# Performance work log

Hardware: AMD Instinct MI355X
Metric: run time of the kernel (lower is better)

## Reference

```python
import jax, jax.numpy as jnp
import numpy as np

WIN = (7, 7)
SHIFT = (3, 3)
HEADS = 12


def _rel_index():
    wh, ww = WIN
    coords = np.stack(np.meshgrid(np.arange(wh), np.arange(ww), indexing='ij')).reshape(2, -1)
    rel = (coords[:, :, None] - coords[:, None, :]).transpose(1, 2, 0).astype(np.int64)
    rel[:, :, 0] += wh - 1
    rel[:, :, 1] += ww - 1
    rel[:, :, 0] *= 2 * ww - 1
    return rel.sum(-1).reshape(-1)  # [N*N]


def _attn_mask(pH, pW, sh, sw):
    wh, ww = WIN
    mask = np.zeros((pH, pW), np.float32)
    h_sl = [(0, pH - wh), (pH - wh, pH - sh), (pH - sh, pH)]
    w_sl = [(0, pW - ww), (pW - ww, pW - sw), (pW - sw, pW)]
    cnt = 0
    for hs in h_sl:
        for ws in w_sl:
            mask[hs[0]:hs[1], ws[0]:ws[1]] = cnt
            cnt += 1
    nw = (pH // wh) * (pW // ww)
    mask = mask.reshape(pH // wh, wh, pW // ww, ww).transpose(0, 2, 1, 3).reshape(nw, wh * ww)
    diff = mask[:, None, :] - mask[:, :, None]
    return jnp.asarray(np.where(diff != 0, -100.0, 0.0).astype(np.float32))  # [nw, N, N]


def setup_inputs() -> dict:
    key = jax.random.key(0)
    ks = jax.random.split(key, 6)
    C = 384
    return {
        'x': jax.random.normal(ks[0], (16, 56, 56, C), jnp.float32),
        'qkv_weight': jax.random.normal(ks[1], (3 * C, C), jnp.float32) * 0.02,
        'qkv_bias': jax.random.normal(ks[2], (3 * C,), jnp.float32) * 0.02,
        'proj_weight': jax.random.normal(ks[3], (C, C), jnp.float32) * 0.02,
        'proj_bias': jax.random.normal(ks[4], (C,), jnp.float32) * 0.02,
        'rel_table': jax.random.normal(ks[5], (169, HEADS), jnp.float32) * 0.02,
    }


def reference(x, qkv_weight, qkv_bias, proj_weight, proj_bias, rel_table):
    B, H, W, C = x.shape
    wh, ww = WIN
    pad_b = (wh - H % wh) % wh
    pad_r = (ww - W % ww) % ww
    xp = jnp.pad(x, ((0, 0), (0, pad_b), (0, pad_r), (0, 0)))
    pH, pW = H + pad_b, W + pad_r
    sh = 0 if wh >= pH else SHIFT[0]
    sw = 0 if ww >= pW else SHIFT[1]
    shifted = (sh + sw) > 0
    if shifted:
        xp = jnp.roll(xp, (-sh, -sw), axis=(1, 2))
    nwh, nww = pH // wh, pW // ww
    nw, N = nwh * nww, wh * ww
    # window partition -> [B*nw, N, C]
    xw = xp.reshape(B, nwh, wh, nww, ww, C).transpose(0, 1, 3, 2, 4, 5).reshape(B * nw, N, C)
    qkv = xw @ qkv_weight.T + qkv_bias
    qkv = qkv.reshape(B * nw, N, 3, HEADS, C // HEADS).transpose(2, 0, 3, 1, 4)
    q, k, v = qkv[0], qkv[1], qkv[2]  # [B*nw, heads, N, hd]
    q = q * (C // HEADS) ** -0.5
    attn = jnp.einsum('whnd,whmd->whnm', q, k)
    bias = rel_table[jnp.asarray(_rel_index())].reshape(N, N, HEADS).transpose(2, 0, 1)
    attn = attn + bias[None]
    if shifted:
        mask = _attn_mask(pH, pW, sh, sw)  # [nw, N, N]
        attn = (attn.reshape(B, nw, HEADS, N, N) + mask[None, :, None]).reshape(B * nw, HEADS, N, N)
    attn = jax.nn.softmax(attn, axis=-1)
    out = jnp.einsum('whnm,whmd->whnd', attn, v).transpose(0, 2, 1, 3).reshape(B * nw, N, C)
    out = out @ proj_weight.T + proj_bias
    out = out.reshape(B, nwh, nww, wh, ww, C).transpose(0, 1, 3, 2, 4, 5).reshape(B, pH, pW, C)
    if shifted:
        out = jnp.roll(out, (sh, sw), axis=(1, 2))
    return out[:, :H, :W, :]
```

## Files before the change

kernel.cpp:

```cpp
#include <hip/hip_runtime.h>

#define CCH 384
#define NHEADS 12
#define HDIM 32
#define NTOK 49
#define NWIN 1024
#define MROWS 50176
#define PSTR 72

typedef __attribute__((ext_vector_type(8))) short bf16x8;
typedef __attribute__((ext_vector_type(4))) float f32x4;

#define WAITVM_BAR(N) asm volatile("s_waitcnt vmcnt(" #N ")\n\ts_barrier" ::: "memory")
#define BAR() asm volatile("s_barrier" ::: "memory")

__device__ __forceinline__ unsigned short f2bf(float f) {
    unsigned u = __builtin_bit_cast(unsigned, f);
    u += 0x7FFFu + ((u >> 16) & 1u);
    return (unsigned short)(u >> 16);
}

__device__ __forceinline__ void g2lds16(const unsigned short* g, unsigned short* l) {
    __builtin_amdgcn_global_load_lds(
        (const __attribute__((address_space(1))) unsigned int*)g,
        (__attribute__((address_space(3))) unsigned int*)l,
        16, 0, 0);
}

__global__ void prep_kernel(const float* __restrict__ qkvw, const float* __restrict__ projw,
                            const float* __restrict__ rel_table,
                            unsigned short* __restrict__ wq, unsigned short* __restrict__ wp,
                            float* __restrict__ btt2) {
    int i = blockIdx.x * 256 + threadIdx.x;
    if (i < 3 * CCH * CCH) wq[i] = f2bf(qkvw[i]);
    if (i < CCH * CCH) wp[i] = f2bf(projw[i]);
    if (i < 4 * NHEADS * 16 * 64) {
        int cls = i / (NHEADS * 16 * 64);
        int rem = i - cls * (NHEADS * 16 * 64);
        int h = rem / (16 * 64);
        int rem2 = rem - h * (16 * 64);
        int rb = rem2 >> 6, cj = rem2 & 63;
        int jreg = 0;
        if (cj < NTOK) {
            int jy = cj / 7, jx = cj - jy * 7;
            int ry = (cls & 2) ? ((jy < 4) ? 1 : 2) : 0;
            int rx = (cls & 1) ? ((jx < 4) ? 1 : 2) : 0;
            jreg = ry * 3 + rx;
        }
        float4 o;
        float* po = (float*)&o;
#pragma unroll
        for (int rr = 0; rr < 4; ++rr) {
            int ri = rb * 4 + rr;
            float v = -1e30f;
            if (ri < NTOK && cj < NTOK) {
                int iy = ri / 7, ix = ri - iy * 7;
                int jy = cj / 7, jx = cj - jy * 7;
                int idx = (iy - jy + 6) * 13 + (ix - jx + 6);
                v = rel_table[idx * NHEADS + h];
                int ry = (cls & 2) ? ((iy < 4) ? 1 : 2) : 0;
                int rx = (cls & 1) ? ((ix < 4) ? 1 : 2) : 0;
                if (ry * 3 + rx != jreg) v -= 100.f;
            }
            po[rr] = v;
        }
        *(float4*)&btt2[(size_t)i * 4] = o;
    }
}

__device__ __forceinline__ size_t row_to_pixel(int r) {
    int wlin = r / 49, n = r - wlin * 49;
    int b = wlin >> 6, wimg = wlin & 63;
    int wy = wimg >> 3, wx = wimg & 7;
    int iy = n / 7, ix = n - iy * 7;
    int y = wy * 7 + iy + 3; if (y >= 56) y -= 56;
    int x = wx * 7 + ix + 3; if (x >= 56) x -= 56;
    return (size_t)((b * 56 + y) * 56 + x);
}

__global__ __launch_bounds__(256) void gather_kernel(const float* __restrict__ xin,
                                                     unsigned short* __restrict__ xw) {
    int idx = blockIdx.x * 256 + threadIdx.x;
    int row = idx / 96, c4 = (idx - row * 96) * 4;
    const float4 v = *(const float4*)(xin + row_to_pixel(row) * CCH + c4);
    ushort4 o;
    o.x = f2bf(v.x); o.y = f2bf(v.y); o.z = f2bf(v.z); o.w = f2bf(v.w);
    *(ushort4*)(xw + (size_t)row * CCH + c4) = o;
}

__global__ __launch_bounds__(512) void qkv_gemm(const unsigned short* __restrict__ xw,
        const unsigned short* __restrict__ wq, const float* __restrict__ qkv_bias,
        unsigned short* __restrict__ qb, unsigned short* __restrict__ kb,
        unsigned short* __restrict__ vb) {
    __shared__ unsigned short As[2][256 * 32];
    __shared__ unsigned short Bs[2][128 * 32];
    const int tid = threadIdx.x;
    const int bid = blockIdx.x;
    const int xcd = bid & 7;
    const int base = (xcd < 4) ? xcd * 221 : (4 * 221 + (xcd - 4) * 220);
    const int swz = base + (bid >> 3);
    const int rb = swz / 9, cb = swz - rb * 9;
    const int row0 = rb * 256;
    const int col0 = cb * 128;
    const int lane = tid & 63, wv = tid >> 6;
    const int wm = wv >> 1, wn = wv & 1;
    const int l15 = lane & 15, g = lane >> 4;

    const int lrow = lane >> 2;
    const int scs = (lane & 3) * 8;
    const unsigned short* gA0 = xw + (size_t)(row0 + wv * 32 + lrow) * CCH + scs;
    const unsigned short* gA1 = gA0 + (size_t)16 * CCH;
    const unsigned short* gB0 = wq + (size_t)(col0 + wv * 16 + lrow) * CCH + scs;

    f32x4 acc[4][4];
#pragma unroll
    for (int i = 0; i < 4; ++i)
#pragma unroll
        for (int j = 0; j < 4; ++j) acc[i][j] = (f32x4){0.f, 0.f, 0.f, 0.f};

    g2lds16(gA0, &As[0][wv * 1024]);
    g2lds16(gA1, &As[0][wv * 1024 + 512]);
    g2lds16(gB0, &Bs[0][wv * 512]);

#pragma unroll
    for (int kk = 0; kk < 12; ++kk) {
        const int cur = kk & 1;
        if (kk < 11) {
            const int nxt = cur ^ 1;
            g2lds16(gA0 + (kk + 1) * 32, &As[nxt][wv * 1024]);
            g2lds16(gA1 + (kk + 1) * 32, &As[nxt][wv * 1024 + 512]);
            g2lds16(gB0 + (kk + 1) * 32, &Bs[nxt][wv * 512]);
            WAITVM_BAR(3);
        } else {
            WAITVM_BAR(0);
        }
        bf16x8 af[4], bfv[4];
#pragma unroll
        for (int mt = 0; mt < 4; ++mt)
            af[mt] = *(const bf16x8*)&As[cur][(wm * 64 + mt * 16 + l15) * 32 + g * 8];
#pragma unroll
        for (int nt = 0; nt < 4; ++nt)
            bfv[nt] = *(const bf16x8*)&Bs[cur][(wn * 64 + nt * 16 + l15) * 32 + g * 8];
#pragma unroll
        for (int mt = 0; mt < 4; ++mt)
#pragma unroll
            for (int nt = 0; nt < 4; ++nt)
                acc[mt][nt] = __builtin_amdgcn_mfma_f32_16x16x32_bf16(af[mt], bfv[nt], acc[mt][nt], 0, 0, 0);
        BAR();
    }

    const float SCALE = 0.17677669529663687f;
#pragma unroll
    for (int nt = 0; nt < 4; ++nt) {
        int col = col0 + wn * 64 + nt * 16 + l15;
        float bias = qkv_bias[col];
        int which = col / CCH;
        int rem = col - which * CCH;
        int h = rem >> 5, d = rem & 31;
        unsigned short* dstb = (which == 0) ? qb : ((which == 1) ? kb : vb);
        float scl = (which == 0) ? SCALE : 1.0f;
#pragma unroll
        for (int mt = 0; mt < 4; ++mt) {
#pragma unroll
            for (int rr = 0; rr < 4; ++rr) {
                int row = row0 + wm * 64 + mt * 16 + g * 4 + rr;
                int w2 = row / 49, n2 = row - w2 * 49;
                size_t inst = (size_t)(w2 * NHEADS + h);
                float v = (acc[mt][nt][rr] + bias) * scl;
                dstb[(inst * NTOK + n2) * HDIM + d] = f2bf(v);
            }
        }
    }
}

__global__ __launch_bounds__(256) void attn_kernel(const unsigned short* __restrict__ qbuf,
        const unsigned short* __restrict__ kbuf, const unsigned short* __restrict__ vbuf,
        const float* __restrict__ btt2, unsigned short* __restrict__ ao) {
    __shared__ unsigned short Ps[4][64 * PSTR];
    __shared__ unsigned short Vt[4][32 * 64];
    const int tid = threadIdx.x;
    const int lane = tid & 63, wv = tid >> 6;
    const int inst = blockIdx.x * 4 + wv;
    const int w = inst / NHEADS, h = inst - w * NHEADS;
    const int l15 = lane & 15, g = lane >> 4;
    const unsigned short* qp = qbuf + (size_t)inst * (NTOK * HDIM);
    const unsigned short* kp = kbuf + (size_t)inst * (NTOK * HDIM);
    const unsigned short* vp = vbuf + (size_t)inst * (NTOK * HDIM);

    const bf16x8 zero8 = {0, 0, 0, 0, 0, 0, 0, 0};
    bf16x8 vpre[4];
#pragma unroll
    for (int p = 0; p < 4; ++p) {
        int e0 = (p * 64 + lane) * 8;
        int tok = e0 >> 5;
        vpre[p] = (tok < NTOK) ? *(const bf16x8*)&vp[e0] : zero8;
    }

    bf16x8 aq[4], bk[4];
#pragma unroll
    for (int mt = 0; mt < 4; ++mt) {
        int row = mt * 16 + l15;
        aq[mt] = (row < NTOK) ? *(const bf16x8*)&qp[row * HDIM + g * 8] : zero8;
    }
#pragma unroll
    for (int nt = 0; nt < 4; ++nt) {
        int colk = nt * 16 + l15;
        bk[nt] = (colk < NTOK) ? *(const bf16x8*)&kp[colk * HDIM + g * 8] : zero8;
    }
    f32x4 s[4][4];
#pragma unroll
    for (int mt = 0; mt < 4; ++mt)
#pragma unroll
        for (int nt = 0; nt < 4; ++nt)
            s[mt][nt] = __builtin_amdgcn_mfma_f32_16x16x32_bf16(aq[mt], bk[nt], (f32x4){0.f, 0.f, 0.f, 0.f}, 0, 0, 0);

    {
        unsigned short* vt = Vt[wv];
#pragma unroll
        for (int p = 0; p < 4; ++p) {
            int e0 = (p * 64 + lane) * 8;
            int tok = e0 >> 5, d0 = e0 & 31;
#pragma unroll
            for (int j = 0; j < 8; ++j) {
                int d = d0 + j;
                vt[d * 64 + (tok ^ ((d & 7) << 3))] = (unsigned short)vpre[p][j];
            }
        }
    }

    const int wimg = w & 63;
    const int wy = wimg >> 3, wx = wimg & 7;
    const int wcls = (((wy == 7) ? 2 : 0) | ((wx == 7) ? 1 : 0));
    const float4* bt4 = (const float4*)btt2 + ((size_t)(wcls * NHEADS + h)) * (16 * 64);

    float inv[4][4];
#pragma unroll
    for (int mt = 0; mt < 4; ++mt) {
        float4 bias4[4];
#pragma unroll
        for (int nt = 0; nt < 4; ++nt)
            bias4[nt] = bt4[(mt * 4 + g) * 64 + nt * 16 + l15];
#pragma unroll
        for (int rr = 0; rr < 4; ++rr) {
#pragma unroll
            for (int nt = 0; nt < 4; ++nt) {
                float bb = (rr == 0) ? bias4[nt].x : (rr == 1) ? bias4[nt].y : (rr == 2) ? bias4[nt].z : bias4[nt].w;
                s[mt][nt][rr] += bb;
            }
            float m = fmaxf(fmaxf(s[mt][0][rr], s[mt][1][rr]), fmaxf(s[mt][2][rr], s[mt][3][rr]));
            m = fmaxf(m, __shfl_xor(m, 1));
            m = fmaxf(m, __shfl_xor(m, 2));
            m = fmaxf(m, __shfl_xor(m, 4));
            m = fmaxf(m, __shfl_xor(m, 8));
            float sum = 0.f;
#pragma unroll
            for (int nt = 0; nt < 4; ++nt) {
                float p = __expf(s[mt][nt][rr] - m);
                s[mt][nt][rr] = p;
                sum += p;
            }
            sum += __shfl_xor(sum, 1);
            sum += __shfl_xor(sum, 2);
            sum += __shfl_xor(sum, 4);
            sum += __shfl_xor(sum, 8);
            inv[mt][rr] = 1.0f / sum;
        }
    }
    unsigned short* ps = Ps[wv];
#pragma unroll
    for (int mt = 0; mt < 4; ++mt)
#pragma unroll
        for (int nt = 0; nt < 4; ++nt)
#pragma unroll
            for (int rr = 0; rr < 4; ++rr)
                ps[(mt * 16 + g * 4 + rr) * PSTR + nt * 16 + l15] = f2bf(s[mt][nt][rr]);

    f32x4 o[4][2];
#pragma unroll
    for (int mt = 0; mt < 4; ++mt)
#pragma unroll
        for (int dt = 0; dt < 2; ++dt) o[mt][dt] = (f32x4){0.f, 0.f, 0.f, 0.f};

    const unsigned short* vt = Vt[wv];
#pragma unroll
    for (int kt = 0; kt < 2; ++kt) {
        bf16x8 ap[4];
#pragma unroll
        for (int mt = 0; mt < 4; ++mt)
            ap[mt] = *(const bf16x8*)&ps[(mt * 16 + l15) * PSTR + kt * 32 + g * 8];
#pragma unroll
        for (int dt = 0; dt < 2; ++dt) {
            const int d = dt * 16 + l15;
            const int cb = kt * 32 + g * 8;
            bf16x8 bv = *(const bf16x8*)&vt[d * 64 + (cb ^ ((d & 7) << 3))];
#pragma unroll
            for (int mt = 0; mt < 4; ++mt)
                o[mt][dt] = __builtin_amdgcn_mfma_f32_16x16x32_bf16(ap[mt], bv, o[mt][dt], 0, 0, 0);
        }
    }
#pragma unroll
    for (int mt = 0; mt < 4; ++mt)
#pragma unroll
        for (int dt = 0; dt < 2; ++dt)
#pragma unroll
            for (int rr = 0; rr < 4; ++rr) {
                int row = mt * 16 + g * 4 + rr;
                if (row < NTOK) {
                    float val = o[mt][dt][rr] * inv[mt][rr];
                    ao[((size_t)(w * NTOK + row)) * CCH + h * HDIM + dt * 16 + l15] = f2bf(val);
                }
            }
}

__global__ __launch_bounds__(256) void proj_gemm(const unsigned short* __restrict__ ain,
        const unsigned short* __restrict__ wp, const float* __restrict__ proj_bias,
        float* __restrict__ out) {
    __shared__ unsigned short As[2][128 * 32];
    __shared__ unsigned short Bs[2][128 * 32];
    const int tid = threadIdx.x;
    const int row0 = blockIdx.x * 128;
    const int col0 = blockIdx.y * 128;
    const int lane = tid & 63, wv = tid >> 6;
    const int wm = wv >> 1, wn = wv & 1;
    const int l15 = lane & 15, g = lane >> 4;

    const int srow = wv * 16 + (lane >> 2);
    const int scs = (lane & 3) * 8;
    const unsigned short* gA0 = ain + (size_t)(row0 + srow) * CCH + scs;
    const unsigned short* gA1 = gA0 + (size_t)64 * CCH;
    const unsigned short* gB0 = wp + (size_t)(col0 + srow) * CCH + scs;
    const unsigned short* gB1 = gB0 + (size_t)64 * CCH;

    f32x4 acc[4][4];
#pragma unroll
    for (int i = 0; i < 4; ++i)
#pragma unroll
        for (int j = 0; j < 4; ++j) acc[i][j] = (f32x4){0.f, 0.f, 0.f, 0.f};

    g2lds16(gA0, &As[0][wv * 512]);
    g2lds16(gA1, &As[0][wv * 512 + 2048]);
    g2lds16(gB0, &Bs[0][wv * 512]);
    g2lds16(gB1, &Bs[0][wv * 512 + 2048]);

#pragma unroll
    for (int kk = 0; kk < 12; ++kk) {
        const int cur = kk & 1;
        if (kk < 11) {
            const int nxt = cur ^ 1;
            g2lds16(gA0 + (kk + 1) * 32, &As[nxt][wv * 512]);
            g2lds16(gA1 + (kk + 1) * 32, &As[nxt][wv * 512 + 2048]);
            g2lds16(gB0 + (kk + 1) * 32, &Bs[nxt][wv * 512]);
            g2lds16(gB1 + (kk + 1) * 32, &Bs[nxt][wv * 512 + 2048]);
            WAITVM_BAR(4);
        } else {
            WAITVM_BAR(0);
        }
        bf16x8 af[4], bfv[4];
#pragma unroll
        for (int mt = 0; mt < 4; ++mt)
            af[mt] = *(const bf16x8*)&As[cur][(wm * 64 + mt * 16 + l15) * 32 + g * 8];
#pragma unroll
        for (int nt = 0; nt < 4; ++nt)
            bfv[nt] = *(const bf16x8*)&Bs[cur][(wn * 64 + nt * 16 + l15) * 32 + g * 8];
#pragma unroll
        for (int mt = 0; mt < 4; ++mt)
#pragma unroll
            for (int nt = 0; nt < 4; ++nt)
                acc[mt][nt] = __builtin_amdgcn_mfma_f32_16x16x32_bf16(af[mt], bfv[nt], acc[mt][nt], 0, 0, 0);
        BAR();
    }
#pragma unroll
    for (int nt = 0; nt < 4; ++nt) {
        int col = col0 + wn * 64 + nt * 16 + l15;
        float bias = proj_bias[col];
#pragma unroll
        for (int mt = 0; mt < 4; ++mt) {
#pragma unroll
            for (int rr = 0; rr < 4; ++rr) {
                int row = row0 + wm * 64 + mt * 16 + g * 4 + rr;
                out[row_to_pixel(row) * CCH + col] = acc[mt][nt][rr] + bias;
            }
        }
    }
}

extern "C" void kernel_launch(void* const* d_in, const int* in_sizes, int n_in,
                              void* d_out, int out_size, void* d_ws, size_t ws_size,
                              hipStream_t stream) {
    const float* x     = (const float*)d_in[0];
    const float* qkvw  = (const float*)d_in[1];
    const float* qkvb  = (const float*)d_in[2];
    const float* projw = (const float*)d_in[3];
    const float* projb = (const float*)d_in[4];
    const float* rel   = (const float*)d_in[5];
    float* out = (float*)d_out;

    char* ws = (char*)d_ws;
    unsigned short* wqb = (unsigned short*)(ws);
    unsigned short* wpb = (unsigned short*)(ws + 884736);
    float* btt2         = (float*)(ws + 884736 + 294912);
    const size_t off  = 2097152;
    const size_t bufb = 38535168ull;
    unsigned short* qb  = (unsigned short*)(ws + off);
    unsigned short* kb  = (unsigned short*)(ws + off + bufb);
    unsigned short* vb  = (unsigned short*)(ws + off + 2 * bufb);
    unsigned short* ao  = (unsigned short*)(ws + off + 3 * bufb);
    unsigned short* xw  = ao;

    prep_kernel<<<1728, 256, 0, stream>>>(qkvw, projw, rel, wqb, wpb, btt2);
    gather_kernel<<<18816, 256, 0, stream>>>(x, xw);
    qkv_gemm<<<1764, 512, 0, stream>>>(xw, wqb, qkvb, qb, kb, vb);
    attn_kernel<<<3072, 256, 0, stream>>>(qb, kb, vb, btt2, ao);
    proj_gemm<<<dim3(392, 3), 256, 0, stream>>>(ao, wpb, projb, out);
}
```

Before: 174.4 us.

## Fuse window gather and bf16 conversion into QKV GEMM; swizzle LDS tiles

Removes the separate gather kernel. The QKV GEMM now loads fp32 x directly at the shifted-window pixel addresses, converts it to bf16 in registers and stores it to LDS, with register prefetch of the next k-tile. An XOR swizzle is added to the LDS layouts of both GEMMs to reduce bank conflicts on the fragment reads. This saves a full bf16 write and reread of the activations plus one launch. In exchange, the A operand is read as fp32 (twice the bytes per tile), goes through registers instead of direct global-to-LDS loads, and each k step waits on vmcnt(0) before its barrier.

```diff
diff --git a/kernel.cpp b/kernel.cpp
--- a/kernel.cpp
+++ b/kernel.cpp
@@ -12,6 +12,7 @@
 typedef __attribute__((ext_vector_type(4))) float f32x4;
 
 #define WAITVM_BAR(N) asm volatile("s_waitcnt vmcnt(" #N ")\n\ts_barrier" ::: "memory")
+#define WAITALL_BAR() asm volatile("s_waitcnt vmcnt(0) lgkmcnt(0)\n\ts_barrier" ::: "memory")
 #define BAR() asm volatile("s_barrier" ::: "memory")
 
 __device__ __forceinline__ unsigned short f2bf(float f) {
@@ -25,6 +26,15 @@
         (const __attribute__((address_space(1))) unsigned int*)g,
         (__attribute__((address_space(3))) unsigned int*)l,
         16, 0, 0);
+}
+
+__device__ __forceinline__ void st8(unsigned short* p, float4 a, float4 b) {
+    bf16x8 v;
+    v[0] = (short)f2bf(a.x); v[1] = (short)f2bf(a.y);
+    v[2] = (short)f2bf(a.z); v[3] = (short)f2bf(a.w);
+    v[4] = (short)f2bf(b.x); v[5] = (short)f2bf(b.y);
+    v[6] = (short)f2bf(b.z); v[7] = (short)f2bf(b.w);
+    *(bf16x8*)p = v;
 }
 
 __global__ void prep_kernel(const float* __restrict__ qkvw, const float* __restrict__ projw,
@@ -78,17 +88,7 @@
     return (size_t)((b * 56 + y) * 56 + x);
 }
 
-__global__ __launch_bounds__(256) void gather_kernel(const float* __restrict__ xin,
-                                                     unsigned short* __restrict__ xw) {
-    int idx = blockIdx.x * 256 + threadIdx.x;
-    int row = idx / 96, c4 = (idx - row * 96) * 4;
-    const float4 v = *(const float4*)(xin + row_to_pixel(row) * CCH + c4);
-    ushort4 o;
-    o.x = f2bf(v.x); o.y = f2bf(v.y); o.z = f2bf(v.z); o.w = f2bf(v.w);
-    *(ushort4*)(xw + (size_t)row * CCH + c4) = o;
-}
-
-__global__ __launch_bounds__(512) void qkv_gemm(const unsigned short* __restrict__ xw,
+__global__ __launch_bounds__(512) void qkv_gemm(const float* __restrict__ xin,
         const unsigned short* __restrict__ wq, const float* __restrict__ qkv_bias,
         unsigned short* __restrict__ qb, unsigned short* __restrict__ kb,
         unsigned short* __restrict__ vb) {
@@ -107,10 +107,17 @@
     const int l15 = lane & 15, g = lane >> 4;
 
     const int lrow = lane >> 2;
-    const int scs = (lane & 3) * 8;
-    const unsigned short* gA0 = xw + (size_t)(row0 + wv * 32 + lrow) * CCH + scs;
-    const unsigned short* gA1 = gA0 + (size_t)16 * CCH;
-    const unsigned short* gB0 = wq + (size_t)(col0 + wv * 16 + lrow) * CCH + scs;
+    const int lc = lane & 3;
+    const int rA = wv * 32 + lrow;
+    const int rB = wv * 16 + lrow;
+    const int fA = (rA >> 1) & 3;
+    const int fB = (rB >> 1) & 3;
+    const float* gA0 = xin + row_to_pixel(row0 + rA) * CCH + lc * 8;
+    const float* gA1 = xin + row_to_pixel(row0 + rA + 16) * CCH + lc * 8;
+    const int wA0 = rA * 32 + (lc ^ fA) * 8;
+    const int wA1 = (rA + 16) * 32 + (lc ^ fA) * 8;
+    const unsigned short* gB0 = wq + (size_t)(col0 + rB) * CCH + ((lc ^ fB) * 8);
+    const int rc = (g ^ ((l15 >> 1) & 3)) * 8;
 
     f32x4 acc[4][4];
 #pragma unroll
@@ -118,35 +125,44 @@
 #pragma unroll
         for (int j = 0; j < 4; ++j) acc[i][j] = (f32x4){0.f, 0.f, 0.f, 0.f};
 
-    g2lds16(gA0, &As[0][wv * 1024]);
-    g2lds16(gA1, &As[0][wv * 1024 + 512]);
+    float4 a0 = *(const float4*)(gA0);
+    float4 a1 = *(const float4*)(gA0 + 4);
+    float4 a2 = *(const float4*)(gA1);
+    float4 a3 = *(const float4*)(gA1 + 4);
     g2lds16(gB0, &Bs[0][wv * 512]);
+    st8(&As[0][wA0], a0, a1);
+    st8(&As[0][wA1], a2, a3);
+    WAITALL_BAR();
 
 #pragma unroll
     for (int kk = 0; kk < 12; ++kk) {
         const int cur = kk & 1;
+        const int nxt = cur ^ 1;
         if (kk < 11) {
-            const int nxt = cur ^ 1;
-            g2lds16(gA0 + (kk + 1) * 32, &As[nxt][wv * 1024]);
-            g2lds16(gA1 + (kk + 1) * 32, &As[nxt][wv * 1024 + 512]);
+            a0 = *(const float4*)(gA0 + (kk + 1) * 32);
+            a1 = *(const float4*)(gA0 + (kk + 1) * 32 + 4);
+            a2 = *(const float4*)(gA1 + (kk + 1) * 32);
+            a3 = *(const float4*)(gA1 + (kk + 1) * 32 + 4);
             g2lds16(gB0 + (kk + 1) * 32, &Bs[nxt][wv * 512]);
-            WAITVM_BAR(3);
-        } else {
-            WAITVM_BAR(0);
-        }
+        }
+        __builtin_amdgcn_sched_barrier(0);
         bf16x8 af[4], bfv[4];
 #pragma unroll
         for (int mt = 0; mt < 4; ++mt)
-            af[mt] = *(const bf16x8*)&As[cur][(wm * 64 + mt * 16 + l15) * 32 + g * 8];
+            af[mt] = *(const bf16x8*)&As[cur][(wm * 64 + mt * 16 + l15) * 32 + rc];
 #pragma unroll
         for (int nt = 0; nt < 4; ++nt)
-            bfv[nt] = *(const bf16x8*)&Bs[cur][(wn * 64 + nt * 16 + l15) * 32 + g * 8];
+            bfv[nt] = *(const bf16x8*)&Bs[cur][(wn * 64 + nt * 16 + l15) * 32 + rc];
 #pragma unroll
         for (int mt = 0; mt < 4; ++mt)
 #pragma unroll
             for (int nt = 0; nt < 4; ++nt)
                 acc[mt][nt] = __builtin_amdgcn_mfma_f32_16x16x32_bf16(af[mt], bfv[nt], acc[mt][nt], 0, 0, 0);
-        BAR();
+        if (kk < 11) {
+            st8(&As[nxt][wA0], a0, a1);
+            st8(&As[nxt][wA1], a2, a3);
+            WAITALL_BAR();
+        }
     }
 
     const float SCALE = 0.17677669529663687f;
@@ -325,11 +341,12 @@
     const int l15 = lane & 15, g = lane >> 4;
 
     const int srow = wv * 16 + (lane >> 2);
-    const int scs = (lane & 3) * 8;
+    const int scs = (((lane & 3) ^ ((srow >> 1) & 3)) * 8);
     const unsigned short* gA0 = ain + (size_t)(row0 + srow) * CCH + scs;
     const unsigned short* gA1 = gA0 + (size_t)64 * CCH;
     const unsigned short* gB0 = wp + (size_t)(col0 + srow) * CCH + scs;
     const unsigned short* gB1 = gB0 + (size_t)64 * CCH;
+    const int rc = (g ^ ((l15 >> 1) & 3)) * 8;
 
     f32x4 acc[4][4];
 #pragma unroll
@@ -358,10 +375,10 @@
         bf16x8 af[4], bfv[4];
 #pragma unroll
         for (int mt = 0; mt < 4; ++mt)
-            af[mt] = *(const bf16x8*)&As[cur][(wm * 64 + mt * 16 + l15) * 32 + g * 8];
+            af[mt] = *(const bf16x8*)&As[cur][(wm * 64 + mt * 16 + l15) * 32 + rc];
 #pragma unroll
         for (int nt = 0; nt < 4; ++nt)
-            bfv[nt] = *(const bf16x8*)&Bs[cur][(wn * 64 + nt * 16 + l15) * 32 + g * 8];
+            bfv[nt] = *(const bf16x8*)&Bs[cur][(wn * 64 + nt * 16 + l15) * 32 + rc];
 #pragma unroll
         for (int mt = 0; mt < 4; ++mt)
 #pragma unroll
@@ -405,11 +422,9 @@
     unsigned short* kb  = (unsigned short*)(ws + off + bufb);
     unsigned short* vb  = (unsigned short*)(ws + off + 2 * bufb);
     unsigned short* ao  = (unsigned short*)(ws + off + 3 * bufb);
-    unsigned short* xw  = ao;
 
     prep_kernel<<<1728, 256, 0, stream>>>(qkvw, projw, rel, wqb, wpb, btt2);
-    gather_kernel<<<18816, 256, 0, stream>>>(x, xw);
-    qkv_gemm<<<1764, 512, 0, stream>>>(xw, wqb, qkvb, qb, kb, vb);
+    qkv_gemm<<<1764, 512, 0, stream>>>(x, wqb, qkvb, qb, kb, vb);
     attn_kernel<<<3072, 256, 0, stream>>>(qb, kb, vb, btt2, ao);
     proj_gemm<<<dim3(392, 3), 256, 0, stream>>>(ao, wpb, projb, out);
 }
```

Result: slower. 232.9 us (+33.5%).
